# Kernel tuning notes

Hardware: AMD Instinct MI355X
Metric: run time of the kernel (lower is better)

The kernel has to match this reference:

```python
import jax, jax.numpy as jnp
import numpy as np

BATCH = 8192
IN_FEATURES = 1024
OUT_FEATURES = 1024
GRID_SIZE = 5
SPLINE_ORDER = 3
GRID_MIN, GRID_MAX = -1.0, 1.0
NUM_BASES = GRID_SIZE + SPLINE_ORDER  # 8
GRID_LEN = GRID_SIZE + 2 * SPLINE_ORDER + 1  # 12


def setup_inputs() -> dict:
    key = jax.random.key(0)
    k1, k2, k3 = jax.random.split(key, 3)
    x = jax.random.normal(k1, (BATCH, IN_FEATURES), dtype=jnp.float32)
    base_weight = jax.random.normal(k2, (OUT_FEATURES, IN_FEATURES), dtype=jnp.float32) * 0.1
    spline_weight = jax.random.normal(k3, (OUT_FEATURES, IN_FEATURES, NUM_BASES), dtype=jnp.float32) * 0.1
    grid = jnp.linspace(GRID_MIN, GRID_MAX, GRID_LEN, dtype=jnp.float32)  # buffer, not learned
    return {"x": x, "base_weight": base_weight, "spline_weight": spline_weight, "grid": grid}


def _bspline_basis(xc, grid, order):
    """Iterative Cox-de Boor DP, vectorized over all features and basis indices.
    xc: [B, F] clamped inputs; grid: [G] uniform knots (all denominators > 0).
    Returns [B, F, G - order - 1] = [B, F, NUM_BASES]."""
    G = grid.shape[0]
    xe = xc[..., None]  # [B, F, 1]
    # k = 0: indicator of knot interval, matches (x >= grid[i]) & (x < grid[i+1])
    B = ((xe >= grid[:-1]) & (xe < grid[1:])).astype(xc.dtype)  # [B, F, G-1]
    for k in range(1, order + 1):
        left = (xe - grid[: G - k - 1]) / (grid[k : G - 1] - grid[: G - k - 1]) * B[..., :-1]
        right = (grid[k + 1 : G] - xe) / (grid[k + 1 : G] - grid[1 : G - k]) * B[..., 1:]
        B = left + right  # [B, F, G-1-k]
    return B


def reference(x, base_weight, spline_weight, grid):
    # base path: SiLU activation then linear
    base_output = jax.nn.silu(x) @ base_weight.T  # [B, out]
    # spline path: B-spline basis per feature, weighted sum over (in, basis)
    x_clamped = jnp.clip(x, GRID_MIN * 0.99, GRID_MAX * 0.99)
    basis = _bspline_basis(x_clamped, grid, SPLINE_ORDER)  # [B, in, NUM_BASES]
    spline_output = jnp.einsum("bin,oin->bo", basis, spline_weight)
    return base_output + spline_output
```

## Files before the change

kernel.cpp:

```cpp
#include <hip/hip_runtime.h>
#include <stdint.h>

typedef _Float16 f16;
typedef __attribute__((ext_vector_type(8))) _Float16 f16x8;
typedef __attribute__((ext_vector_type(4))) float f32x4;

#define BATCH 8192
#define INF   1024
#define OUTF  1024
#define KTOT  9216
#define NT    72

__device__ __forceinline__ void gload16(const void* g, void* l) {
  __builtin_amdgcn_global_load_lds(
      (const __attribute__((address_space(1))) uint32_t*)g,
      (__attribute__((address_space(3))) uint32_t*)l, 16, 0, 0);
}

__global__ __launch_bounds__(256) void convert_w_kernel(
    const float* __restrict__ bw, const float* __restrict__ sw,
    f16* __restrict__ Wb)
{
  int idx = blockIdx.x * 256 + threadIdx.x;
  int o = idx / 1152;
  int r = idx - o * 1152;
  int k8 = r * 8;
  const float* src = (k8 < INF) ? (bw + (size_t)o * INF + k8)
                                : (sw + (size_t)o * (INF * 8) + (k8 - INF));
  float4 v0 = *(const float4*)src;
  float4 v1 = *(const float4*)(src + 4);
  f16x8 ov;
  ov[0] = (f16)v0.x; ov[1] = (f16)v0.y; ov[2] = (f16)v0.z; ov[3] = (f16)v0.w;
  ov[4] = (f16)v1.x; ov[5] = (f16)v1.y; ov[6] = (f16)v1.z; ov[7] = (f16)v1.w;
  *(f16x8*)(Wb + (size_t)o * KTOT + k8) = ov;
}

__global__ __launch_bounds__(256) void prep_a_kernel(
    const float* __restrict__ x, const float* __restrict__ grid,
    f16* __restrict__ Abuf)
{
  int q = blockIdx.x * 256 + threadIdx.x;
  int b = q >> 8;
  int i0 = (q & 255) << 2;
  float4 xv = *(const float4*)(x + ((size_t)b << 10) + i0);
  float xa[4] = {xv.x, xv.y, xv.z, xv.w};

  float g[12];
#pragma unroll
  for (int j = 0; j < 12; ++j) g[j] = grid[j];
  float H  = g[1] - g[0];
  float r1 = 1.0f / H;
  float r2 = 0.5f * r1;
  float r3 = (1.0f / 3.0f) * r1;

  f16 sil[4];
  f16x8 bas[4];
#pragma unroll
  for (int e = 0; e < 4; ++e) {
    float v = xa[e];
    sil[e] = (f16)(v / (1.0f + __expf(-v)));
    float xe = fminf(fmaxf(v, -0.99f), 0.99f);
    float Bv[11];
#pragma unroll
    for (int j = 0; j < 11; ++j) Bv[j] = (xe >= g[j] && xe < g[j + 1]) ? 1.0f : 0.0f;
#pragma unroll
    for (int j = 0; j < 10; ++j) Bv[j] = (xe - g[j]) * r1 * Bv[j] + (g[j + 2] - xe) * r1 * Bv[j + 1];
#pragma unroll
    for (int j = 0; j < 9; ++j)  Bv[j] = (xe - g[j]) * r2 * Bv[j] + (g[j + 3] - xe) * r2 * Bv[j + 1];
#pragma unroll
    for (int j = 0; j < 8; ++j)  Bv[j] = (xe - g[j]) * r3 * Bv[j] + (g[j + 4] - xe) * r3 * Bv[j + 1];
#pragma unroll
    for (int n = 0; n < 8; ++n) bas[e][n] = (f16)Bv[n];
  }
  f16* row = Abuf + (size_t)b * KTOT;
  *(uint64_t*)(row + i0) = *(const uint64_t*)sil;
  f16* bp = row + INF + (size_t)i0 * 8;
#pragma unroll
  for (int e = 0; e < 4; ++e) *(f16x8*)(bp + e * 8) = bas[e];
}

#define LDA(base, m, s) (*(const f16x8*)((base) + ((wr*128 + (m)*16 + la) * 64 + ((((s)*4 + lb) ^ lasw) * 8))))
#define LDB(base, n, s) (*(const f16x8*)((base) + ((wcn*64 + (n)*16 + la) * 64 + ((((s)*4 + lb) ^ lasw) * 8))))

#define MFMA1(m, n, s) acc[m][n] = __builtin_amdgcn_mfma_f32_16x16x32_f16(af[m][s], bf[n][s], acc[m][n], 0, 0, 0)
#define MFMA_ROW(m) do { \
  MFMA1(m,0,0); MFMA1(m,0,1); MFMA1(m,1,0); MFMA1(m,1,1); \
  MFMA1(m,2,0); MFMA1(m,2,1); MFMA1(m,3,0); MFMA1(m,3,1); } while (0)

#define LGKM0 do { asm volatile("s_waitcnt lgkmcnt(0)" ::: "memory"); \
                   __builtin_amdgcn_sched_barrier(0); } while (0)
#define SBAR  __builtin_amdgcn_s_barrier()
#define SCHED0 __builtin_amdgcn_sched_barrier(0)

__global__ __launch_bounds__(512, 2) void kan_gemm_kernel(
    const f16* __restrict__ A, const f16* __restrict__ W,
    float* __restrict__ C)
{
  __shared__ __align__(16) f16 lsA[2 * 256 * 64];
  __shared__ __align__(16) f16 lsB[2 * 256 * 64];

  const size_t K = KTOT;
  int bid = blockIdx.x;
  int wg  = (bid & 7) * 32 + (bid >> 3);
  int tm  = wg & 31;
  int gg  = wg >> 5;
  int tn  = gg >> 1;
  size_t kbase = (size_t)(gg & 1) * (NT * 64);

  int tid = threadIdx.x;
  int w = tid >> 6, l = tid & 63;
  int wr = w >> 2, wcn = w & 3;
  int la = l & 15, lb = l >> 4, lasw = la & 7;

  int rh = tid >> 3;
  int sc = (tid & 7) ^ (rh & 7);
  const f16* aSrc0 = A + (size_t)(tm * 256 + rh) * K + kbase + sc * 8;
  const f16* bSrc0 = W + (size_t)(tn * 256 + rh) * K + kbase + sc * 8;

  auto stage = [&](int h) {
    if (h >= 4 * NT) return;
    int tile = h >> 2, ty = h & 3, half = ty & 1;
    size_t koff = (size_t)tile * 64;
    if (ty < 2) {
      const f16* s = aSrc0 + (size_t)half * 128 * K + koff;
      f16* d = lsA + (tile & 1) * 16384 + half * 8192 + w * 512;
      gload16(s, d);
      gload16(s + 64 * K, d + 4096);
    } else {
      const f16* s = bSrc0 + (size_t)half * 128 * K + koff;
      f16* d = lsB + (tile & 1) * 16384 + half * 8192 + w * 512;
      gload16(s, d);
      gload16(s + 64 * K, d + 4096);
    }
  };

  f16x8 af[8][2], bf[4][2];
  f32x4 acc[8][4] = {};

  stage(2); stage(3); stage(0); stage(1); stage(6); stage(7);
  asm volatile("s_waitcnt vmcnt(4)" ::: "memory");
  SBAR; SCHED0;
  {
    const f16* bA = lsA; const f16* bB = lsB;
#pragma unroll
    for (int n = 0; n < 4; ++n) { bf[n][0] = LDB(bB, n, 0); bf[n][1] = LDB(bB, n, 1); }
    af[0][0] = LDA(bA, 0, 0); af[0][1] = LDA(bA, 0, 1);
    af[1][0] = LDA(bA, 1, 0); af[1][1] = LDA(bA, 1, 1);
  }

  for (int t = 0; t < NT; ++t) {
    const f16* bA  = lsA + (t & 1) * 16384;
    const f16* bB  = lsB + (t & 1) * 16384;
    const f16* bA1 = lsA + ((t + 1) & 1) * 16384;
    const f16* bB1 = lsB + ((t + 1) & 1) * 16384;
    int h1 = 4 * (t + 1), h2 = 4 * (t + 2);

    stage(h1 + 0);
    SCHED0; SBAR; LGKM0;
    __builtin_amdgcn_s_setprio(1);
    MFMA_ROW(0); MFMA_ROW(1);
    __builtin_amdgcn_s_setprio(0);
    af[2][0] = LDA(bA, 2, 0); af[2][1] = LDA(bA, 2, 1);
    af[3][0] = LDA(bA, 3, 0); af[3][1] = LDA(bA, 3, 1);
    SCHED0; SBAR;

    stage(h1 + 1);
    stage(h2 + 2);
    SCHED0; SBAR; LGKM0;
    __builtin_amdgcn_s_setprio(1);
    MFMA_ROW(2); MFMA_ROW(3);
    __builtin_amdgcn_s_setprio(0);
    af[4][0] = LDA(bA, 4, 0); af[4][1] = LDA(bA, 4, 1);
    af[5][0] = LDA(bA, 5, 0); af[5][1] = LDA(bA, 5, 1);
    SCHED0; SBAR;

    stage(h2 + 3);
    SCHED0; SBAR; LGKM0;
    __builtin_amdgcn_s_setprio(1);
    MFMA_ROW(4); MFMA_ROW(5);
    __builtin_amdgcn_s_setprio(0);
    af[6][0] = LDA(bA, 6, 0); af[6][1] = LDA(bA, 6, 1);
    af[7][0] = LDA(bA, 7, 0); af[7][1] = LDA(bA, 7, 1);
    SCHED0; SBAR;

    if (t < NT - 2)       asm volatile("s_waitcnt vmcnt(4)" ::: "memory");
    else if (t == NT - 2) asm volatile("s_waitcnt vmcnt(0)" ::: "memory");
    SCHED0; SBAR; LGKM0;
    __builtin_amdgcn_s_setprio(1);
    MFMA_ROW(6); MFMA_ROW(7);
    __builtin_amdgcn_s_setprio(0);
    if (t < NT - 1) {
#pragma unroll
      for (int n = 0; n < 4; ++n) { bf[n][0] = LDB(bB1, n, 0); bf[n][1] = LDB(bB1, n, 1); }
      af[0][0] = LDA(bA1, 0, 0); af[0][1] = LDA(bA1, 0, 1);
      af[1][0] = LDA(bA1, 1, 0); af[1][1] = LDA(bA1, 1, 1);
    }
    SCHED0; SBAR;
  }

  int rowBase = tm * 256 + wr * 128 + lb * 4;
  int colBase = tn * 256 + wcn * 64 + la;
#pragma unroll
  for (int m = 0; m < 8; ++m)
#pragma unroll
    for (int n = 0; n < 4; ++n) {
      int col = colBase + n * 16;
#pragma unroll
      for (int j = 0; j < 4; ++j) {
        int row = rowBase + m * 16 + j;
        atomicAdd(&C[(size_t)row * OUTF + col], acc[m][n][j]);
      }
    }
}

extern "C" void kernel_launch(void* const* d_in, const int* in_sizes, int n_in,
                              void* d_out, int out_size, void* d_ws, size_t ws_size,
                              hipStream_t stream)
{
  const float* x  = (const float*)d_in[0];
  const float* bw = (const float*)d_in[1];
  const float* sw = (const float*)d_in[2];
  const float* gr = (const float*)d_in[3];
  float* out = (float*)d_out;

  f16* Wb = (f16*)d_ws;
  size_t wBytes = (size_t)OUTF * KTOT * sizeof(f16);
  f16* Abuf = (f16*)((char*)d_ws + wBytes);

  convert_w_kernel<<<(OUTF * (KTOT / 8)) / 256, 256, 0, stream>>>(bw, sw, Wb);
  prep_a_kernel<<<(BATCH * INF / 4) / 256, 256, 0, stream>>>(x, gr, Abuf);
  hipMemsetAsync(d_out, 0, (size_t)out_size * sizeof(float), stream);
  kan_gemm_kernel<<<256, 512, 0, stream>>>(Abuf, Wb, out);
}
```

Measured before the change: 246.1 us.

## Replace split-K atomics with partial buffer plus reduce, reorder MFMA issue

The split-K GEMM now writes each half's partial sums with plain stores, one half to the output and the other to a workspace buffer, and a separate vectorized kernel adds them. This removes the memset and the fp32 atomicAdd epilogue, which in the old code sent scattered atomic traffic to 8M output elements. The MFMA sequence is regrouped by k-slice across two rows, and two stage loads are now issued together at the start of each iteration. It costs an extra 32MB workspace buffer plus a reduce pass reading and writing 64MB, and falls back to the atomic path when the workspace is too small.

New measurement: 218.6 us. 1.13x faster.

```diff
diff --git a/kernel.cpp b/kernel.cpp
--- a/kernel.cpp
+++ b/kernel.cpp
@@ -83,18 +83,22 @@
 #define LDB(base, n, s) (*(const f16x8*)((base) + ((wcn*64 + (n)*16 + la) * 64 + ((((s)*4 + lb) ^ lasw) * 8))))
 
 #define MFMA1(m, n, s) acc[m][n] = __builtin_amdgcn_mfma_f32_16x16x32_f16(af[m][s], bf[n][s], acc[m][n], 0, 0, 0)
-#define MFMA_ROW(m) do { \
-  MFMA1(m,0,0); MFMA1(m,0,1); MFMA1(m,1,0); MFMA1(m,1,1); \
-  MFMA1(m,2,0); MFMA1(m,2,1); MFMA1(m,3,0); MFMA1(m,3,1); } while (0)
+#define MFMA_PHASE(m0) do { \
+  MFMA1(m0,0,0);   MFMA1(m0,1,0);   MFMA1(m0,2,0);   MFMA1(m0,3,0); \
+  MFMA1(m0+1,0,0); MFMA1(m0+1,1,0); MFMA1(m0+1,2,0); MFMA1(m0+1,3,0); \
+  MFMA1(m0,0,1);   MFMA1(m0,1,1);   MFMA1(m0,2,1);   MFMA1(m0,3,1); \
+  MFMA1(m0+1,0,1); MFMA1(m0+1,1,1); MFMA1(m0+1,2,1); MFMA1(m0+1,3,1); \
+} while (0)
 
 #define LGKM0 do { asm volatile("s_waitcnt lgkmcnt(0)" ::: "memory"); \
                    __builtin_amdgcn_sched_barrier(0); } while (0)
 #define SBAR  __builtin_amdgcn_s_barrier()
 #define SCHED0 __builtin_amdgcn_sched_barrier(0)
 
+template <bool ATOMIC>
 __global__ __launch_bounds__(512, 2) void kan_gemm_kernel(
     const f16* __restrict__ A, const f16* __restrict__ W,
-    float* __restrict__ C)
+    float* __restrict__ C, float* __restrict__ P1)
 {
   __shared__ __align__(16) f16 lsA[2 * 256 * 64];
   __shared__ __align__(16) f16 lsB[2 * 256 * 64];
@@ -105,7 +109,8 @@
   int tm  = wg & 31;
   int gg  = wg >> 5;
   int tn  = gg >> 1;
-  size_t kbase = (size_t)(gg & 1) * (NT * 64);
+  int split = gg & 1;
+  size_t kbase = (size_t)split * (NT * 64);
 
   int tid = threadIdx.x;
   int w = tid >> 6, l = tid & 63;
@@ -155,20 +160,19 @@
     const f16* bB1 = lsB + ((t + 1) & 1) * 16384;
     int h1 = 4 * (t + 1), h2 = 4 * (t + 2);
 
-    stage(h1 + 0);
-    SCHED0; SBAR; LGKM0;
-    __builtin_amdgcn_s_setprio(1);
-    MFMA_ROW(0); MFMA_ROW(1);
+    stage(h1 + 0); stage(h1 + 1);
+    SCHED0; SBAR; LGKM0;
+    __builtin_amdgcn_s_setprio(1);
+    MFMA_PHASE(0);
     __builtin_amdgcn_s_setprio(0);
     af[2][0] = LDA(bA, 2, 0); af[2][1] = LDA(bA, 2, 1);
     af[3][0] = LDA(bA, 3, 0); af[3][1] = LDA(bA, 3, 1);
     SCHED0; SBAR;
 
-    stage(h1 + 1);
     stage(h2 + 2);
     SCHED0; SBAR; LGKM0;
     __builtin_amdgcn_s_setprio(1);
-    MFMA_ROW(2); MFMA_ROW(3);
+    MFMA_PHASE(2);
     __builtin_amdgcn_s_setprio(0);
     af[4][0] = LDA(bA, 4, 0); af[4][1] = LDA(bA, 4, 1);
     af[5][0] = LDA(bA, 5, 0); af[5][1] = LDA(bA, 5, 1);
@@ -177,7 +181,7 @@
     stage(h2 + 3);
     SCHED0; SBAR; LGKM0;
     __builtin_amdgcn_s_setprio(1);
-    MFMA_ROW(4); MFMA_ROW(5);
+    MFMA_PHASE(4);
     __builtin_amdgcn_s_setprio(0);
     af[6][0] = LDA(bA, 6, 0); af[6][1] = LDA(bA, 6, 1);
     af[7][0] = LDA(bA, 7, 0); af[7][1] = LDA(bA, 7, 1);
@@ -187,7 +191,7 @@
     else if (t == NT - 2) asm volatile("s_waitcnt vmcnt(0)" ::: "memory");
     SCHED0; SBAR; LGKM0;
     __builtin_amdgcn_s_setprio(1);
-    MFMA_ROW(6); MFMA_ROW(7);
+    MFMA_PHASE(6);
     __builtin_amdgcn_s_setprio(0);
     if (t < NT - 1) {
 #pragma unroll
@@ -200,6 +204,7 @@
 
   int rowBase = tm * 256 + wr * 128 + lb * 4;
   int colBase = tn * 256 + wcn * 64 + la;
+  float* dst = ATOMIC ? C : (split ? P1 : C);
 #pragma unroll
   for (int m = 0; m < 8; ++m)
 #pragma unroll
@@ -208,9 +213,20 @@
 #pragma unroll
       for (int j = 0; j < 4; ++j) {
         int row = rowBase + m * 16 + j;
-        atomicAdd(&C[(size_t)row * OUTF + col], acc[m][n][j]);
+        if (ATOMIC) atomicAdd(&C[(size_t)row * OUTF + col], acc[m][n][j]);
+        else        dst[(size_t)row * OUTF + col] = acc[m][n][j];
       }
     }
+}
+
+__global__ __launch_bounds__(256) void reduce_kernel(
+    float* __restrict__ out, const float* __restrict__ p)
+{
+  size_t i = ((size_t)blockIdx.x * 256 + threadIdx.x) * 4;
+  f32x4 a = *(f32x4*)(out + i);
+  f32x4 b = *(const f32x4*)(p + i);
+  a += b;
+  *(f32x4*)(out + i) = a;
 }
 
 extern "C" void kernel_launch(void* const* d_in, const int* in_sizes, int n_in,
@@ -226,9 +242,18 @@
   f16* Wb = (f16*)d_ws;
   size_t wBytes = (size_t)OUTF * KTOT * sizeof(f16);
   f16* Abuf = (f16*)((char*)d_ws + wBytes);
+  size_t aBytes = (size_t)BATCH * KTOT * sizeof(f16);
+  size_t oBytes = (size_t)BATCH * OUTF * sizeof(float);
 
   convert_w_kernel<<<(OUTF * (KTOT / 8)) / 256, 256, 0, stream>>>(bw, sw, Wb);
   prep_a_kernel<<<(BATCH * INF / 4) / 256, 256, 0, stream>>>(x, gr, Abuf);
-  hipMemsetAsync(d_out, 0, (size_t)out_size * sizeof(float), stream);
-  kan_gemm_kernel<<<256, 512, 0, stream>>>(Abuf, Wb, out);
-}
+
+  if (ws_size >= wBytes + aBytes + oBytes) {
+    float* P1 = (float*)((char*)d_ws + wBytes + aBytes);
+    kan_gemm_kernel<false><<<256, 512, 0, stream>>>(Abuf, Wb, out, P1);
+    reduce_kernel<<<(int)(oBytes / sizeof(float) / 4 / 256), 256, 0, stream>>>(out, P1);
+  } else {
+    hipMemsetAsync(d_out, 0, oBytes, stream);
+    kan_gemm_kernel<true><<<256, 512, 0, stream>>>(Abuf, Wb, out, nullptr);
+  }
+}
```
